# Optimization experiments

Measured on AMD Instinct MI355X. Metric: run time of the kernel, lower is better.

## Reference

```python
import jax, jax.numpy as jnp
import numpy as np

N = 50000
E = 800000
IN = 128
HID = 32
HEADS = 4
OUT = 32
NEG_SLOPE = 0.2  # PyG GATConv default


def setup_inputs() -> dict:
    key = jax.random.key(0)
    ks = jax.random.split(key, 16)
    s = lambda k, sh: jax.random.normal(k, sh, jnp.float32) * 0.05
    inp = {}
    inp["x"] = jax.random.normal(ks[0], (N, IN), jnp.float32)
    inp["edge_idx"] = jax.random.randint(ks[1], (2, E), 0, N)
    inp["edge_attr"] = jax.random.normal(ks[2], (E, 1), jnp.float32)
    inp["lin1_w"] = s(ks[3], (IN, HEADS * HID))
    inp["att1_src"] = s(ks[4], (HEADS, HID))
    inp["att1_dst"] = s(ks[5], (HEADS, HID))
    inp["lin1_edge_w"] = s(ks[6], (1, HEADS * HID))
    inp["att1_edge"] = s(ks[7], (HEADS, HID))
    inp["bias1"] = jnp.zeros((HEADS * HID,), jnp.float32)
    inp["lin2_w"] = s(ks[8], (HEADS * HID, OUT))
    inp["att2_src"] = s(ks[9], (1, OUT))
    inp["att2_dst"] = s(ks[10], (1, OUT))
    inp["lin2_edge_w"] = s(ks[11], (1, OUT))
    inp["att2_edge"] = s(ks[12], (1, OUT))
    inp["bias2"] = jnp.zeros((OUT,), jnp.float32)
    return inp


def _gat_conv(x, src, dst, eattr, lin_w, a_src, a_dst, lin_e, a_e, bias, heads, ch, concat):
    """PyG GATConv (eval mode): gather -> leaky_relu logits -> segment softmax over dst -> scatter-sum."""
    n = x.shape[0]
    xl = (x @ lin_w).reshape(n, heads, ch)                      # [N,H,C]
    alpha = ((xl * a_src).sum(-1)[src]                          # [Etot,H]
             + (xl * a_dst).sum(-1)[dst]
             + ((eattr @ lin_e).reshape(-1, heads, ch) * a_e).sum(-1))
    alpha = jax.nn.leaky_relu(alpha, NEG_SLOPE)
    amax = jax.ops.segment_max(alpha, dst, num_segments=n)      # every node has a self-loop
    ex = jnp.exp(alpha - amax[dst])
    den = jax.ops.segment_sum(ex, dst, num_segments=n)
    w = ex / den[dst]                                           # [Etot,H]
    out = jax.ops.segment_sum(w[:, :, None] * xl[src], dst, num_segments=n)  # [N,H,C]
    out = out.reshape(n, heads * ch) if concat else out.mean(axis=1)
    return out + bias


def reference(x, edge_idx, edge_attr,
              lin1_w, att1_src, att1_dst, lin1_edge_w, att1_edge, bias1,
              lin2_w, att2_src, att2_dst, lin2_edge_w, att2_edge, bias2):
    n = x.shape[0]
    # add_self_loops=True with edge_attr fill_value='mean' (PyG default when edge_dim is set)
    loops = jnp.arange(n)
    src = jnp.concatenate([edge_idx[0], loops])
    dst = jnp.concatenate([edge_idx[1], loops])
    ea = jnp.concatenate(
        [edge_attr, jnp.broadcast_to(edge_attr.mean(0, keepdims=True), (n, edge_attr.shape[1]))], 0)
    h = jax.nn.elu(_gat_conv(x, src, dst, ea, lin1_w, att1_src, att1_dst,
                             lin1_edge_w, att1_edge, bias1, HEADS, HID, True))
    # F.dropout with training=False -> identity (eval mode)
    return _gat_conv(h, src, dst, ea, lin2_w, att2_src, att2_dst,
                     lin2_edge_w, att2_edge, bias2, 1, OUT, True)
```

## Files before the change

### kernel.cpp

```cpp
#include <hip/hip_runtime.h>
#include <hip/hip_fp16.h>
#include <math.h>

#define NN   50000
#define EE   800000
#define ETOT 850000
#define NEG  0.2f
#define SCAN_BLOCKS ((NN + 255) / 256)

#define O_DEG    0
#define O_EASUM  50000
#define ZERO_ELEMS 50004
#define O_COEF   50004
#define O_ROWPTR 50012
#define O_CURSOR 100016
#define O_BLKSUM 150016
#define O_BLKOFF 150272
#define O_CSRSRC 150528
#define O_EASLOT 1000528
#define O_ASRC1  1850528
#define O_ADST1  2050528
#define O_XLH    2250528
#define O_OUT1   5450528
#define O_HLH    11850528
#define O_ASRC2  12650528
#define O_ADST2  12700528
#define WS_ELEMS 12750528

__global__ void k_ea_count(const float* __restrict__ ea, const int* __restrict__ ei,
                           float* __restrict__ easum, int* __restrict__ deg) {
  __shared__ float red[4];
  float s = 0.f;
  int stride = gridDim.x * blockDim.x;
  for (int i = blockIdx.x * blockDim.x + threadIdx.x; i < EE; i += stride) {
    s += ea[i];
    atomicAdd(deg + ei[EE + i], 1);
  }
  #pragma unroll
  for (int o = 32; o > 0; o >>= 1) s += __shfl_down(s, o, 64);
  if ((threadIdx.x & 63) == 0) red[threadIdx.x >> 6] = s;
  __syncthreads();
  if (threadIdx.x == 0) atomicAdd(easum, red[0] + red[1] + red[2] + red[3]);
}

__device__ __forceinline__ int wave_incl_scan(int v, int lane) {
  #pragma unroll
  for (int o = 1; o < 64; o <<= 1) {
    int u = __shfl_up(v, o, 64);
    if (lane >= o) v += u;
  }
  return v;
}

__global__ __launch_bounds__(256) void k_scan_blk(const int* __restrict__ deg,
                                                  int* __restrict__ rowptr,
                                                  int* __restrict__ blksum) {
  __shared__ int wsum[4];
  const int t = threadIdx.x;
  const int i = blockIdx.x * 256 + t;
  const int lane = t & 63, wv = t >> 6;
  int v = (i < NN) ? (deg[i] + 1) : 0;
  int incl = wave_incl_scan(v, lane);
  if (lane == 63) wsum[wv] = incl;
  __syncthreads();
  int off = 0;
  #pragma unroll
  for (int k = 0; k < 4; ++k) if (k < wv) off += wsum[k];
  incl += off;
  if (i < NN) rowptr[i] = incl - v;
  if (t == 255) blksum[blockIdx.x] = incl;
}

__global__ __launch_bounds__(256) void k_scan_top(
    const int* __restrict__ blksum, int* __restrict__ blkoff,
    const float* __restrict__ lew1, const float* __restrict__ ae1,
    const float* __restrict__ lew2, const float* __restrict__ ae2,
    float* __restrict__ coef) {
  __shared__ int wsum[4];
  const int t = threadIdx.x;
  const int lane = t & 63, wv = t >> 6;
  int v = (t < SCAN_BLOCKS) ? blksum[t] : 0;
  int incl = wave_incl_scan(v, lane);
  if (lane == 63) wsum[wv] = incl;
  __syncthreads();
  int off = 0;
  #pragma unroll
  for (int k = 0; k < 4; ++k) if (k < wv) off += wsum[k];
  incl += off;
  if (t < SCAN_BLOCKS) blkoff[t] = incl - v;
  if (t < 128) {
    float p = lew1[t] * ae1[t];
    #pragma unroll
    for (int o = 16; o > 0; o >>= 1) p += __shfl_down(p, o, 32);
    if ((t & 31) == 0) coef[t >> 5] = p;
    if (t < 32) {
      float q = lew2[t] * ae2[t];
      #pragma unroll
      for (int o = 16; o > 0; o >>= 1) q += __shfl_down(q, o, 32);
      if (t == 0) coef[4] = q;
    }
  }
}

__global__ __launch_bounds__(256) void k_scan_add(
    int* __restrict__ rowptr, int* __restrict__ cursor,
    const int* __restrict__ blkoff, const int* __restrict__ deg,
    const float* __restrict__ easum,
    int* __restrict__ csr_src, float* __restrict__ ea_slot) {
  const int i = blockIdx.x * 256 + threadIdx.x;
  if (i < NN) {
    int r = rowptr[i] + blkoff[blockIdx.x];
    rowptr[i] = r;
    cursor[i] = r;
    int slot = r + deg[i];
    csr_src[slot] = i;
    ea_slot[slot] = easum[0] * (1.f / EE);
  }
  if (i == 0) rowptr[NN] = ETOT;
}

#define GEMM_STEP(WB, K, XS) {                                              \
    const float4* Wr = (const float4*)((WB) + (size_t)(K));                 \
    _Pragma("unroll")                                                       \
    for (int j4 = 0; j4 < 8; ++j4) {                                        \
      float4 wv = Wr[j4];                                                   \
      acc[j4 * 4 + 0] += (XS) * wv.x;                                       \
      acc[j4 * 4 + 1] += (XS) * wv.y;                                       \
      acc[j4 * 4 + 2] += (XS) * wv.z;                                       \
      acc[j4 * 4 + 3] += (XS) * wv.w;                                       \
    } }

#define L1_NB ((NN + 63) / 64)
#define LIN1B (L1_NB * 4)
#define FILLB ((EE + 63) / 64)
__global__ __launch_bounds__(64) void k_fused(
    const float* __restrict__ x, const float* __restrict__ W,
    const float* __restrict__ att_src, const float* __restrict__ att_dst,
    __half* __restrict__ xlh, float* __restrict__ asrc, float* __restrict__ adst,
    const int* __restrict__ ei, const float* __restrict__ eattr,
    int* __restrict__ cursor, int* __restrict__ csr_src, float* __restrict__ ea_slot) {
  const int bid = blockIdx.x;
  if (bid >= LIN1B) {
    int e = (bid - LIN1B) * 64 + threadIdx.x;
    if (e < EE) {
      int s = ei[e];
      int d = ei[EE + e];
      float ea = eattr[e];
      int slot = atomicAdd(cursor + d, 1);
      csr_src[slot] = s;
      ea_slot[slot] = ea;
    }
    return;
  }
  const int h   = bid / L1_NB;
  const int n   = (bid % L1_NB) * 64 + threadIdx.x;
  const int nc  = n < NN ? n : NN - 1;
  const float4* xr = (const float4*)(x + (size_t)nc * 128);
  const float*  Wh = W + h * 32;
  float acc[32];
  #pragma unroll
  for (int j = 0; j < 32; ++j) acc[j] = 0.f;
  float4 xv = xr[0];
  for (int kt = 0; kt < 32; ++kt) {
    float4 cur = xv;
    if (kt < 31) xv = xr[kt + 1];
    GEMM_STEP(Wh, (kt * 4 + 0) * 128, cur.x);
    GEMM_STEP(Wh, (kt * 4 + 1) * 128, cur.y);
    GEMM_STEP(Wh, (kt * 4 + 2) * 128, cur.z);
    GEMM_STEP(Wh, (kt * 4 + 3) * 128, cur.w);
  }
  if (n < NN) {
    __align__(16) __half hbuf[32];
    #pragma unroll
    for (int j = 0; j < 32; ++j) hbuf[j] = __float2half_rn(acc[j]);
    float4* dst = (float4*)(xlh + (size_t)n * 128 + h * 32);
    #pragma unroll
    for (int i = 0; i < 4; ++i) dst[i] = ((const float4*)hbuf)[i];
    float ss = 0.f, sd = 0.f;
    #pragma unroll
    for (int j = 0; j < 32; ++j) {
      ss += acc[j] * att_src[h * 32 + j];
      sd += acc[j] * att_dst[h * 32 + j];
    }
    asrc[n * 4 + h] = ss;
    adst[n * 4 + h] = sd;
  }
}

__global__ __launch_bounds__(256) void k_agg1(
    const int* __restrict__ rowptr, const int* __restrict__ csr_src,
    const float* __restrict__ ea_slot, const float* __restrict__ asrc,
    const float* __restrict__ adst, const float* __restrict__ coef,
    const __half* __restrict__ xlh, float* __restrict__ out1) {
  int n = blockIdx.x * 8 + (threadIdx.x >> 5);
  if (n >= NN) return;
  int l = threadIdx.x & 31;
  int c4 = l << 2;
  int h = l >> 3;
  float cf = coef[h];
  float ad = adst[(size_t)n * 4 + h];
  int r0 = rowptr[n], r1 = rowptr[n + 1];
  float a0 = 0.f, a1 = 0.f, a2 = 0.f, a3 = 0.f, den = 0.f;
  for (int j = r0; j < r1; j += 4) {
    int sv[4]; float eav[4], asv[4]; uint2 raw[4];
    #pragma unroll
    for (int k = 0; k < 4; ++k) {
      int jj = (j + k < r1) ? (j + k) : (r1 - 1);
      sv[k] = csr_src[jj];
      eav[k] = ea_slot[jj];
    }
    #pragma unroll
    for (int k = 0; k < 4; ++k) {
      asv[k] = asrc[(size_t)sv[k] * 4 + h];
      raw[k] = *(const uint2*)(xlh + (size_t)sv[k] * 128 + c4);
    }
    #pragma unroll
    for (int k = 0; k < 4; ++k) {
      float alpha = asv[k] + ad + eav[k] * cf;
      alpha = alpha > 0.f ? alpha : NEG * alpha;
      float ex = (j + k < r1) ? __expf(alpha) : 0.f;
      __half2 p0, p1;
      *(unsigned int*)&p0 = raw[k].x;
      *(unsigned int*)&p1 = raw[k].y;
      float2 f0 = __half22float2(p0), f1 = __half22float2(p1);
      a0 += ex * f0.x;
      a1 += ex * f0.y;
      a2 += ex * f1.x;
      a3 += ex * f1.y;
      den += ex;
    }
  }
  float inv = 1.f / den;
  *(float4*)(out1 + (size_t)n * 128 + c4) = make_float4(a0 * inv, a1 * inv, a2 * inv, a3 * inv);
}

__global__ __launch_bounds__(64) void k_lin2(
    const float* __restrict__ out1, const float* __restrict__ bias1,
    const float* __restrict__ W2,
    const float* __restrict__ as2w, const float* __restrict__ ad2w,
    __half* __restrict__ hlh, float* __restrict__ asrc2, float* __restrict__ adst2) {
  const int n  = blockIdx.x * 64 + threadIdx.x;
  const int nc = n < NN ? n : NN - 1;
  const float4* xr = (const float4*)(out1 + (size_t)nc * 128);
  const float4* br = (const float4*)bias1;
  float acc[32];
  #pragma unroll
  for (int j = 0; j < 32; ++j) acc[j] = 0.f;
  float4 xv = xr[0];
  for (int kt = 0; kt < 32; ++kt) {
    float4 cur = xv;
    if (kt < 31) xv = xr[kt + 1];
    float4 b = br[kt];
    cur.x += b.x; cur.y += b.y; cur.z += b.z; cur.w += b.w;
    cur.x = cur.x > 0.f ? cur.x : (expf(cur.x) - 1.f);
    cur.y = cur.y > 0.f ? cur.y : (expf(cur.y) - 1.f);
    cur.z = cur.z > 0.f ? cur.z : (expf(cur.z) - 1.f);
    cur.w = cur.w > 0.f ? cur.w : (expf(cur.w) - 1.f);
    GEMM_STEP(W2, (kt * 4 + 0) * 32, cur.x);
    GEMM_STEP(W2, (kt * 4 + 1) * 32, cur.y);
    GEMM_STEP(W2, (kt * 4 + 2) * 32, cur.z);
    GEMM_STEP(W2, (kt * 4 + 3) * 32, cur.w);
  }
  if (n < NN) {
    __align__(16) __half hbuf[32];
    #pragma unroll
    for (int j = 0; j < 32; ++j) hbuf[j] = __float2half_rn(acc[j]);
    float4* dst = (float4*)(hlh + (size_t)n * 32);
    #pragma unroll
    for (int i = 0; i < 4; ++i) dst[i] = ((const float4*)hbuf)[i];
    float ps = 0.f, pd = 0.f;
    #pragma unroll
    for (int j = 0; j < 32; ++j) {
      ps += acc[j] * as2w[j];
      pd += acc[j] * ad2w[j];
    }
    asrc2[n] = ps;
    adst2[n] = pd;
  }
}

__global__ __launch_bounds__(256) void k_agg2(
    const int* __restrict__ rowptr, const int* __restrict__ csr_src,
    const float* __restrict__ ea_slot, const float* __restrict__ asrc2,
    const float* __restrict__ adst2, const float* __restrict__ coef,
    const __half* __restrict__ hlh, const float* __restrict__ bias2,
    float* __restrict__ out) {
  int n = blockIdx.x * 32 + (threadIdx.x >> 3);
  if (n >= NN) return;
  int c4 = (threadIdx.x & 7) << 2;
  float cf = coef[4];
  float ad = adst2[n];
  int r0 = rowptr[n], r1 = rowptr[n + 1];
  float a0 = 0.f, a1 = 0.f, a2 = 0.f, a3 = 0.f, den = 0.f;
  for (int j = r0; j < r1; j += 4) {
    int sv[4]; float eav[4], asv[4]; uint2 raw[4];
    #pragma unroll
    for (int k = 0; k < 4; ++k) {
      int jj = (j + k < r1) ? (j + k) : (r1 - 1);
      sv[k] = csr_src[jj];
      eav[k] = ea_slot[jj];
    }
    #pragma unroll
    for (int k = 0; k < 4; ++k) {
      asv[k] = asrc2[sv[k]];
      raw[k] = *(const uint2*)(hlh + (size_t)sv[k] * 32 + c4);
    }
    #pragma unroll
    for (int k = 0; k < 4; ++k) {
      float alpha = asv[k] + ad + eav[k] * cf;
      alpha = alpha > 0.f ? alpha : NEG * alpha;
      float ex = (j + k < r1) ? __expf(alpha) : 0.f;
      __half2 p0, p1;
      *(unsigned int*)&p0 = raw[k].x;
      *(unsigned int*)&p1 = raw[k].y;
      float2 f0 = __half22float2(p0), f1 = __half22float2(p1);
      a0 += ex * f0.x;
      a1 += ex * f0.y;
      a2 += ex * f1.x;
      a3 += ex * f1.y;
      den += ex;
    }
  }
  float inv = 1.f / den;
  float4 b = *(const float4*)(bias2 + c4);
  *(float4*)(out + (size_t)n * 32 + c4) =
      make_float4(a0 * inv + b.x, a1 * inv + b.y, a2 * inv + b.z, a3 * inv + b.w);
}

extern "C" void kernel_launch(void* const* d_in, const int* in_sizes, int n_in,
                              void* d_out, int out_size, void* d_ws, size_t ws_size,
                              hipStream_t stream) {
  const float* x        = (const float*)d_in[0];
  const int*   ei       = (const int*)d_in[1];
  const float* eattr    = (const float*)d_in[2];
  const float* lin1_w   = (const float*)d_in[3];
  const float* att1_src = (const float*)d_in[4];
  const float* att1_dst = (const float*)d_in[5];
  const float* lin1_ew  = (const float*)d_in[6];
  const float* att1_e   = (const float*)d_in[7];
  const float* bias1    = (const float*)d_in[8];
  const float* lin2_w   = (const float*)d_in[9];
  const float* att2_src = (const float*)d_in[10];
  const float* att2_dst = (const float*)d_in[11];
  const float* lin2_ew  = (const float*)d_in[12];
  const float* att2_e   = (const float*)d_in[13];
  const float* bias2    = (const float*)d_in[14];
  float* out = (float*)d_out;
  float* ws  = (float*)d_ws;
  int*   wsi = (int*)d_ws;

  int*    deg     = wsi + O_DEG;
  float*  easum   = ws + O_EASUM;
  float*  coef    = ws + O_COEF;
  int*    rowptr  = wsi + O_ROWPTR;
  int*    cursor  = wsi + O_CURSOR;
  int*    blksum  = wsi + O_BLKSUM;
  int*    blkoff  = wsi + O_BLKOFF;
  int*    csr_src = wsi + O_CSRSRC;
  float*  ea_slot = ws + O_EASLOT;
  float*  asrc1   = ws + O_ASRC1;
  float*  adst1   = ws + O_ADST1;
  __half* xlh     = (__half*)(ws + O_XLH);
  float*  out1    = ws + O_OUT1;
  __half* hlh     = (__half*)(ws + O_HLH);
  float*  asrc2   = ws + O_ASRC2;
  float*  adst2   = ws + O_ADST2;

  hipMemsetAsync(ws, 0, (size_t)ZERO_ELEMS * sizeof(float), stream);

  k_ea_count<<<256, 256, 0, stream>>>(eattr, ei, easum, deg);

  k_scan_blk<<<SCAN_BLOCKS, 256, 0, stream>>>(deg, rowptr, blksum);
  k_scan_top<<<1, 256, 0, stream>>>(blksum, blkoff, lin1_ew, att1_e, lin2_ew, att2_e, coef);
  k_scan_add<<<SCAN_BLOCKS, 256, 0, stream>>>(rowptr, cursor, blkoff, deg, easum, csr_src, ea_slot);

  k_fused<<<LIN1B + FILLB, 64, 0, stream>>>(x, lin1_w, att1_src, att1_dst, xlh, asrc1, adst1,
                                            ei, eattr, cursor, csr_src, ea_slot);

  k_agg1<<<(NN + 7) / 8, 256, 0, stream>>>(rowptr, csr_src, ea_slot, asrc1, adst1, coef, xlh, out1);

  k_lin2<<<(NN + 63) / 64, 64, 0, stream>>>(out1, bias1, lin2_w, att2_src, att2_dst, hlh, asrc2, adst2);
  k_agg2<<<(NN + 31) / 32, 256, 0, stream>>>(rowptr, csr_src, ea_slot, asrc2, adst2, coef, hlh, bias2, out);
}
```

Before: 316.9 us.

## Fuse agg1 with lin2, single-block scan, and atomic-rank CSR fill

Records each edge's atomic rank during degree counting, so the CSR fill computes slots as rowptr+rank and no longer needs a second round of atomics on a cursor array. The three-kernel scan becomes one 1024-thread single-block kernel. Layer-1 aggregation is fused with the ELU, bias and layer-2 linear projection through shared memory, which removes the out1 round trip to global memory. Edge-fill blocks are interleaved with GEMM blocks, and the serial single-block scan could become a latency bottleneck.

```diff
diff --git a/kernel.cpp b/kernel.cpp
--- a/kernel.cpp
+++ b/kernel.cpp
@@ -6,35 +6,32 @@
 #define EE   800000
 #define ETOT 850000
 #define NEG  0.2f
-#define SCAN_BLOCKS ((NN + 255) / 256)
 
 #define O_DEG    0
 #define O_EASUM  50000
 #define ZERO_ELEMS 50004
 #define O_COEF   50004
 #define O_ROWPTR 50012
-#define O_CURSOR 100016
-#define O_BLKSUM 150016
-#define O_BLKOFF 150272
-#define O_CSRSRC 150528
-#define O_EASLOT 1000528
-#define O_ASRC1  1850528
-#define O_ADST1  2050528
-#define O_XLH    2250528
-#define O_OUT1   5450528
-#define O_HLH    11850528
-#define O_ASRC2  12650528
-#define O_ADST2  12700528
-#define WS_ELEMS 12750528
-
-__global__ void k_ea_count(const float* __restrict__ ea, const int* __restrict__ ei,
-                           float* __restrict__ easum, int* __restrict__ deg) {
+#define O_RANK   100016
+#define O_CSRSRC 900016
+#define O_EASLOT 1750016
+#define O_ASRC1  2600016
+#define O_ADST1  2800016
+#define O_XLH    3000016
+#define O_HLH    6200016
+#define O_ASRC2  7000016
+#define O_ADST2  7050016
+#define WS_ELEMS 7100016
+
+__global__ __launch_bounds__(256) void k_ea_count(
+    const float* __restrict__ ea, const int* __restrict__ ei,
+    float* __restrict__ easum, int* __restrict__ deg, int* __restrict__ rank) {
   __shared__ float red[4];
+  int e = blockIdx.x * 256 + threadIdx.x;
   float s = 0.f;
-  int stride = gridDim.x * blockDim.x;
-  for (int i = blockIdx.x * blockDim.x + threadIdx.x; i < EE; i += stride) {
-    s += ea[i];
-    atomicAdd(deg + ei[EE + i], 1);
+  if (e < EE) {
+    s = ea[e];
+    rank[e] = atomicAdd(deg + ei[EE + e], 1);
   }
   #pragma unroll
   for (int o = 32; o > 0; o >>= 1) s += __shfl_down(s, o, 64);
@@ -52,42 +49,16 @@
   return v;
 }
 
-__global__ __launch_bounds__(256) void k_scan_blk(const int* __restrict__ deg,
-                                                  int* __restrict__ rowptr,
-                                                  int* __restrict__ blksum) {
-  __shared__ int wsum[4];
-  const int t = threadIdx.x;
-  const int i = blockIdx.x * 256 + t;
-  const int lane = t & 63, wv = t >> 6;
-  int v = (i < NN) ? (deg[i] + 1) : 0;
-  int incl = wave_incl_scan(v, lane);
-  if (lane == 63) wsum[wv] = incl;
-  __syncthreads();
-  int off = 0;
-  #pragma unroll
-  for (int k = 0; k < 4; ++k) if (k < wv) off += wsum[k];
-  incl += off;
-  if (i < NN) rowptr[i] = incl - v;
-  if (t == 255) blksum[blockIdx.x] = incl;
-}
-
-__global__ __launch_bounds__(256) void k_scan_top(
-    const int* __restrict__ blksum, int* __restrict__ blkoff,
+#define SCAN_IT 49
+__global__ __launch_bounds__(1024) void k_scan_one(
+    const int* __restrict__ deg, const float* __restrict__ easum,
+    int* __restrict__ rowptr, int* __restrict__ csr_src, float* __restrict__ ea_slot,
     const float* __restrict__ lew1, const float* __restrict__ ae1,
     const float* __restrict__ lew2, const float* __restrict__ ae2,
     float* __restrict__ coef) {
-  __shared__ int wsum[4];
+  __shared__ int wsum[16];
   const int t = threadIdx.x;
   const int lane = t & 63, wv = t >> 6;
-  int v = (t < SCAN_BLOCKS) ? blksum[t] : 0;
-  int incl = wave_incl_scan(v, lane);
-  if (lane == 63) wsum[wv] = incl;
-  __syncthreads();
-  int off = 0;
-  #pragma unroll
-  for (int k = 0; k < 4; ++k) if (k < wv) off += wsum[k];
-  incl += off;
-  if (t < SCAN_BLOCKS) blkoff[t] = incl - v;
   if (t < 128) {
     float p = lew1[t] * ae1[t];
     #pragma unroll
@@ -100,23 +71,31 @@
       if (t == 0) coef[4] = q;
     }
   }
-}
-
-__global__ __launch_bounds__(256) void k_scan_add(
-    int* __restrict__ rowptr, int* __restrict__ cursor,
-    const int* __restrict__ blkoff, const int* __restrict__ deg,
-    const float* __restrict__ easum,
-    int* __restrict__ csr_src, float* __restrict__ ea_slot) {
-  const int i = blockIdx.x * 256 + threadIdx.x;
-  if (i < NN) {
-    int r = rowptr[i] + blkoff[blockIdx.x];
-    rowptr[i] = r;
-    cursor[i] = r;
-    int slot = r + deg[i];
-    csr_src[slot] = i;
-    ea_slot[slot] = easum[0] * (1.f / EE);
-  }
-  if (i == 0) rowptr[NN] = ETOT;
+  const float eamean = easum[0] * (1.f / EE);
+  int carry = 0;
+  int idx = t;
+  int v = (idx < NN) ? deg[idx] + 1 : 0;
+  for (int i = 0; i < SCAN_IT; ++i) {
+    int nidx = idx + 1024;
+    int nv = (i + 1 < SCAN_IT && nidx < NN) ? deg[nidx] + 1 : 0;
+    int incl = wave_incl_scan(v, lane);
+    if (lane == 63) wsum[wv] = incl;
+    __syncthreads();
+    int off = 0, tot = 0;
+    #pragma unroll
+    for (int k = 0; k < 16; ++k) { int w = wsum[k]; tot += w; if (k < wv) off += w; }
+    __syncthreads();
+    if (idx < NN) {
+      int excl = carry + off + incl - v;
+      rowptr[idx] = excl;
+      int slot = excl + (v - 1);
+      csr_src[slot] = idx;
+      ea_slot[slot] = eamean;
+    }
+    carry += tot;
+    idx = nidx; v = nv;
+  }
+  if (t == 0) rowptr[NN] = ETOT;
 }
 
 #define GEMM_STEP(WB, K, XS) {                                              \
@@ -132,28 +111,29 @@
 
 #define L1_NB ((NN + 63) / 64)
 #define LIN1B (L1_NB * 4)
-#define FILLB ((EE + 63) / 64)
 __global__ __launch_bounds__(64) void k_fused(
     const float* __restrict__ x, const float* __restrict__ W,
     const float* __restrict__ att_src, const float* __restrict__ att_dst,
     __half* __restrict__ xlh, float* __restrict__ asrc, float* __restrict__ adst,
     const int* __restrict__ ei, const float* __restrict__ eattr,
-    int* __restrict__ cursor, int* __restrict__ csr_src, float* __restrict__ ea_slot) {
-  const int bid = blockIdx.x;
-  if (bid >= LIN1B) {
-    int e = (bid - LIN1B) * 64 + threadIdx.x;
+    const int* __restrict__ rank, const int* __restrict__ rowptr,
+    int* __restrict__ csr_src, float* __restrict__ ea_slot) {
+  const int g = blockIdx.x / 5;
+  const int r = blockIdx.x % 5;
+  if (r != 0) {
+    int e = (g * 4 + r - 1) * 64 + threadIdx.x;
     if (e < EE) {
       int s = ei[e];
       int d = ei[EE + e];
       float ea = eattr[e];
-      int slot = atomicAdd(cursor + d, 1);
+      int slot = rowptr[d] + rank[e];
       csr_src[slot] = s;
       ea_slot[slot] = ea;
     }
     return;
   }
-  const int h   = bid / L1_NB;
-  const int n   = (bid % L1_NB) * 64 + threadIdx.x;
+  const int h   = g / L1_NB;
+  const int n   = (g % L1_NB) * 64 + threadIdx.x;
   const int nc  = n < NN ? n : NN - 1;
   const float4* xr = (const float4*)(x + (size_t)nc * 128);
   const float*  Wh = W + h * 32;
@@ -187,16 +167,20 @@
   }
 }
 
-__global__ __launch_bounds__(256) void k_agg1(
+__global__ __launch_bounds__(256) void k_agg1lin2(
     const int* __restrict__ rowptr, const int* __restrict__ csr_src,
     const float* __restrict__ ea_slot, const float* __restrict__ asrc,
     const float* __restrict__ adst, const float* __restrict__ coef,
-    const __half* __restrict__ xlh, float* __restrict__ out1) {
-  int n = blockIdx.x * 8 + (threadIdx.x >> 5);
-  if (n >= NN) return;
-  int l = threadIdx.x & 31;
-  int c4 = l << 2;
-  int h = l >> 3;
+    const __half* __restrict__ xlh, const float* __restrict__ bias1,
+    const float* __restrict__ W2,
+    const float* __restrict__ as2w, const float* __restrict__ ad2w,
+    __half* __restrict__ hlh, float* __restrict__ asrc2, float* __restrict__ adst2) {
+  __shared__ float hsh[8][128];
+  const int ni = threadIdx.x >> 5;
+  const int n = blockIdx.x * 8 + ni;
+  const int l = threadIdx.x & 31;
+  const int c4 = l << 2;
+  const int h = l >> 3;
   float cf = coef[h];
   float ad = adst[(size_t)n * 4 + h];
   int r0 = rowptr[n], r1 = rowptr[n + 1];
@@ -231,51 +215,37 @@
     }
   }
   float inv = 1.f / den;
-  *(float4*)(out1 + (size_t)n * 128 + c4) = make_float4(a0 * inv, a1 * inv, a2 * inv, a3 * inv);
-}
-
-__global__ __launch_bounds__(64) void k_lin2(
-    const float* __restrict__ out1, const float* __restrict__ bias1,
-    const float* __restrict__ W2,
-    const float* __restrict__ as2w, const float* __restrict__ ad2w,
-    __half* __restrict__ hlh, float* __restrict__ asrc2, float* __restrict__ adst2) {
-  const int n  = blockIdx.x * 64 + threadIdx.x;
-  const int nc = n < NN ? n : NN - 1;
-  const float4* xr = (const float4*)(out1 + (size_t)nc * 128);
-  const float4* br = (const float4*)bias1;
-  float acc[32];
-  #pragma unroll
-  for (int j = 0; j < 32; ++j) acc[j] = 0.f;
-  float4 xv = xr[0];
-  for (int kt = 0; kt < 32; ++kt) {
-    float4 cur = xv;
-    if (kt < 31) xv = xr[kt + 1];
-    float4 b = br[kt];
-    cur.x += b.x; cur.y += b.y; cur.z += b.z; cur.w += b.w;
-    cur.x = cur.x > 0.f ? cur.x : (expf(cur.x) - 1.f);
-    cur.y = cur.y > 0.f ? cur.y : (expf(cur.y) - 1.f);
-    cur.z = cur.z > 0.f ? cur.z : (expf(cur.z) - 1.f);
-    cur.w = cur.w > 0.f ? cur.w : (expf(cur.w) - 1.f);
-    GEMM_STEP(W2, (kt * 4 + 0) * 32, cur.x);
-    GEMM_STEP(W2, (kt * 4 + 1) * 32, cur.y);
-    GEMM_STEP(W2, (kt * 4 + 2) * 32, cur.z);
-    GEMM_STEP(W2, (kt * 4 + 3) * 32, cur.w);
-  }
-  if (n < NN) {
-    __align__(16) __half hbuf[32];
-    #pragma unroll
-    for (int j = 0; j < 32; ++j) hbuf[j] = __float2half_rn(acc[j]);
-    float4* dst = (float4*)(hlh + (size_t)n * 32);
-    #pragma unroll
-    for (int i = 0; i < 4; ++i) dst[i] = ((const float4*)hbuf)[i];
-    float ps = 0.f, pd = 0.f;
-    #pragma unroll
-    for (int j = 0; j < 32; ++j) {
-      ps += acc[j] * as2w[j];
-      pd += acc[j] * ad2w[j];
-    }
-    asrc2[n] = ps;
-    adst2[n] = pd;
+  float4 b1 = *(const float4*)(bias1 + c4);
+  float v0 = a0 * inv + b1.x;  v0 = v0 > 0.f ? v0 : (__expf(v0) - 1.f);
+  float v1 = a1 * inv + b1.y;  v1 = v1 > 0.f ? v1 : (__expf(v1) - 1.f);
+  float v2 = a2 * inv + b1.z;  v2 = v2 > 0.f ? v2 : (__expf(v2) - 1.f);
+  float v3 = a3 * inv + b1.w;  v3 = v3 > 0.f ? v3 : (__expf(v3) - 1.f);
+  hsh[ni][c4 + 0] = v0;
+  hsh[ni][c4 + 1] = v1;
+  hsh[ni][c4 + 2] = v2;
+  hsh[ni][c4 + 3] = v3;
+  __syncthreads();
+  const float* hrow = hsh[ni];
+  float acc2 = 0.f;
+  #pragma unroll
+  for (int k4 = 0; k4 < 32; ++k4) {
+    float4 hv = *(const float4*)(hrow + k4 * 4);
+    acc2 += hv.x * W2[(k4 * 4 + 0) * 32 + l];
+    acc2 += hv.y * W2[(k4 * 4 + 1) * 32 + l];
+    acc2 += hv.z * W2[(k4 * 4 + 2) * 32 + l];
+    acc2 += hv.w * W2[(k4 * 4 + 3) * 32 + l];
+  }
+  hlh[(size_t)n * 32 + l] = __float2half_rn(acc2);
+  float p = acc2 * as2w[l];
+  float q = acc2 * ad2w[l];
+  #pragma unroll
+  for (int o = 16; o > 0; o >>= 1) {
+    p += __shfl_down(p, o, 32);
+    q += __shfl_down(q, o, 32);
+  }
+  if (l == 0) {
+    asrc2[n] = p;
+    adst2[n] = q;
   }
 }
 
@@ -353,32 +323,30 @@
   float*  easum   = ws + O_EASUM;
   float*  coef    = ws + O_COEF;
   int*    rowptr  = wsi + O_ROWPTR;
-  int*    cursor  = wsi + O_CURSOR;
-  int*    blksum  = wsi + O_BLKSUM;
-  int*    blkoff  = wsi + O_BLKOFF;
+  int*    rank    = wsi + O_RANK;
   int*    csr_src = wsi + O_CSRSRC;
   float*  ea_slot = ws + O_EASLOT;
   float*  asrc1   = ws + O_ASRC1;
   float*  adst1   = ws + O_ADST1;
   __half* xlh     = (__half*)(ws + O_XLH);
-  float*  out1    = ws + O_OUT1;
   __half* hlh     = (__half*)(ws + O_HLH);
   float*  asrc2   = ws + O_ASRC2;
   float*  adst2   = ws + O_ADST2;
 
   hipMemsetAsync(ws, 0, (size_t)ZERO_ELEMS * sizeof(float), stream);
 
-  k_ea_count<<<256, 256, 0, stream>>>(eattr, ei, easum, deg);
-
-  k_scan_blk<<<SCAN_BLOCKS, 256, 0, stream>>>(deg, rowptr, blksum);
-  k_scan_top<<<1, 256, 0, stream>>>(blksum, blkoff, lin1_ew, att1_e, lin2_ew, att2_e, coef);
-  k_scan_add<<<SCAN_BLOCKS, 256, 0, stream>>>(rowptr, cursor, blkoff, deg, easum, csr_src, ea_slot);
-
-  k_fused<<<LIN1B + FILLB, 64, 0, stream>>>(x, lin1_w, att1_src, att1_dst, xlh, asrc1, adst1,
-                                            ei, eattr, cursor, csr_src, ea_slot);
-
-  k_agg1<<<(NN + 7) / 8, 256, 0, stream>>>(rowptr, csr_src, ea_slot, asrc1, adst1, coef, xlh, out1);
-
-  k_lin2<<<(NN + 63) / 64, 64, 0, stream>>>(out1, bias1, lin2_w, att2_src, att2_dst, hlh, asrc2, adst2);
-  k_agg2<<<(NN + 31) / 32, 256, 0, stream>>>(rowptr, csr_src, ea_slot, asrc2, adst2, coef, hlh, bias2, out);
-}
+  k_ea_count<<<(EE + 255) / 256, 256, 0, stream>>>(eattr, ei, easum, deg, rank);
+
+  k_scan_one<<<1, 1024, 0, stream>>>(deg, easum, rowptr, csr_src, ea_slot,
+                                     lin1_ew, att1_e, lin2_ew, att2_e, coef);
+
+  k_fused<<<LIN1B * 5, 64, 0, stream>>>(x, lin1_w, att1_src, att1_dst, xlh, asrc1, adst1,
+                                        ei, eattr, rank, rowptr, csr_src, ea_slot);
+
+  k_agg1lin2<<<NN / 8, 256, 0, stream>>>(rowptr, csr_src, ea_slot, asrc1, adst1, coef,
+                                         xlh, bias1, lin2_w, att2_src, att2_dst,
+                                         hlh, asrc2, adst2);
+
+  k_agg2<<<(NN + 31) / 32, 256, 0, stream>>>(rowptr, csr_src, ea_slot, asrc2, adst2, coef,
+                                             hlh, bias2, out);
+}
```

New measurement: 412.1 us. 30.1% more time.
